# Kernel tuning notes

Hardware: AMD Instinct MI355X
Metric: run time of the kernel (lower is better)

Reference implementation:

```python
import jax, jax.numpy as jnp
import numpy as np

N_NODES = 100000


def _hetero_block(x, ei_t, ei_i, Wt, bt, Wi, bi, Wr, br):
    """ResidualGeneralHeteroConvBlock: per-edge-type linear message passing,
    'add' aggregation for temp_previous, 'mean' for intersects, summed across
    edge types, plus linear residual, ReLU."""
    n = x.shape[0]
    # transform-then-gather (cheaper than per-edge transform)
    ht = x @ Wt + bt                                   # [N, C]
    hi = x @ Wi + bi                                   # [N, C]
    # temp_previous: sum aggregation over incoming edges
    agg_t = jax.ops.segment_sum(ht[ei_t[0]], ei_t[1], num_segments=n)
    # intersects: mean aggregation
    sum_i = jax.ops.segment_sum(hi[ei_i[0]], ei_i[1], num_segments=n)
    cnt = jax.ops.segment_sum(jnp.ones((ei_i.shape[1],), x.dtype), ei_i[1],
                              num_segments=n)
    agg_i = sum_i / jnp.maximum(cnt, 1.0)[:, None]
    return jax.nn.relu(agg_t + agg_i + (x @ Wr + br))


def setup_inputs() -> dict:
    key = jax.random.key(0)
    ks = jax.random.split(key, 12)
    E = 2000000
    d = {
        "x": jax.random.normal(ks[0], (N_NODES, 6), jnp.float32),
        "edge_index_temp": jax.random.randint(ks[1], (2, E), 0, N_NODES),
        "edge_index_inter": jax.random.randint(ks[2], (2, E), 0, N_NODES),
        "W1t": jax.random.normal(ks[3], (6, 32), jnp.float32) * 0.3,
        "b1t": jnp.zeros((32,), jnp.float32),
        "W1i": jax.random.normal(ks[4], (6, 32), jnp.float32) * 0.3,
        "b1i": jnp.zeros((32,), jnp.float32),
        "W1r": jax.random.normal(ks[5], (6, 32), jnp.float32) * 0.3,
        "b1r": jnp.zeros((32,), jnp.float32),
        "W2t": jax.random.normal(ks[6], (32, 32), jnp.float32) * 0.15,
        "b2t": jnp.zeros((32,), jnp.float32),
        "W2i": jax.random.normal(ks[7], (32, 32), jnp.float32) * 0.15,
        "b2i": jnp.zeros((32,), jnp.float32),
        "W2r": jax.random.normal(ks[8], (32, 32), jnp.float32) * 0.15,
        "b2r": jnp.zeros((32,), jnp.float32),
        "Wc": jax.random.normal(ks[9], (32, 7), jnp.float32) * 0.15,
        "bc": jnp.zeros((7,), jnp.float32),
    }
    return d


def reference(x, edge_index_temp, edge_index_inter,
              W1t, b1t, W1i, b1i, W1r, b1r,
              W2t, b2t, W2i, b2i, W2r, b2r, Wc, bc):
    h = _hetero_block(x, edge_index_temp, edge_index_inter,
                      W1t, b1t, W1i, b1i, W1r, b1r)
    h = _hetero_block(h, edge_index_temp, edge_index_inter,
                      W2t, b2t, W2i, b2i, W2r, b2r)
    return h @ Wc + bc  # [N, num_classes]
```

## Files before the change

kernel.cpp:

```cpp
#include <hip/hip_runtime.h>


#define BLK 256
#define RN 512
#define KMAX 256
#define CAP 11264
#define CHUNK 4096

typedef unsigned short us8 __attribute__((ext_vector_type(8)));

__device__ inline unsigned short f2bf(float f) {
  unsigned u = __float_as_uint(f);
  return (unsigned short)((u + 0x7FFFu + ((u >> 16) & 1u)) >> 16);
}
__device__ inline float bf2f(unsigned short h) {
  return __uint_as_float(((unsigned)h) << 16);
}

__global__ __launch_bounds__(BLK) void k_prep(const float* __restrict__ x,
                                              unsigned short* __restrict__ xp,
                                              int* __restrict__ curT,
                                              int* __restrict__ curI, int N,
                                              int K) {
  int gid = blockIdx.x * BLK + threadIdx.x;
  if (gid < K) {
    curT[gid] = gid * CAP;
    curI[gid] = gid * CAP;
  }
  if (gid >= N * 8) return;
  int n = gid >> 3, c = gid & 7;
  xp[gid] = (c < 6) ? f2bf(x[n * 6 + c]) : (unsigned short)0;
}

__global__ __launch_bounds__(BLK) void k_bin3(
    const int* __restrict__ eiT, int ET, int* __restrict__ curT,
    int* __restrict__ binT, const int* __restrict__ eiI, int EI,
    int* __restrict__ curI, int* __restrict__ binI, int K) {
  const int* ei = blockIdx.y ? eiI : eiT;
  int E = blockIdx.y ? EI : ET;
  int* gcur = blockIdx.y ? curI : curT;
  int* binned = blockIdx.y ? binI : binT;
  int cs = blockIdx.x * CHUNK;
  if (cs >= E) return;
  int ce = min(E, cs + CHUNK);
  int cnt = ce - cs;
  __shared__ int ebuf[CHUNK];
  __shared__ unsigned char bbuf[CHUNK];
  __shared__ int hist[KMAX], cur[KMAX], gdelta[KMAX], s[KMAX];
  int t = threadIdx.x;
  hist[t] = 0;
  __syncthreads();
  for (int e = cs + t; e < ce; e += BLK) atomicAdd(&hist[ei[E + e] >> 9], 1);
  __syncthreads();
  int v = hist[t];
  s[t] = v;
  __syncthreads();
  for (int off = 1; off < KMAX; off <<= 1) {
    int x = (t >= off) ? s[t - off] : 0;
    __syncthreads();
    s[t] += x;
    __syncthreads();
  }
  int excl = s[t] - v;
  cur[t] = excl;
  if (t < K) gdelta[t] = atomicAdd(&gcur[t], v) - excl;
  __syncthreads();
  for (int e = cs + t; e < ce; e += BLK) {
    int src = ei[e];
    int d = ei[E + e];
    int b = d >> 9;
    int slot = atomicAdd(&cur[b], 1);
    ebuf[slot] = (src << 9) | (d & 511);
    bbuf[slot] = (unsigned char)b;
  }
  __syncthreads();
  for (int i = t; i < cnt; i += BLK) {
    int b = bbuf[i];
    __builtin_nontemporal_store(ebuf[i], &binned[i + gdelta[b]]);
  }
}

__global__ __launch_bounds__(512) void k_sortcsr4(
    const int* __restrict__ binT, const int* __restrict__ curT,
    unsigned short* __restrict__ csrT, int* __restrict__ startT,
    int* __restrict__ degT, int4* __restrict__ mqT,
    const int* __restrict__ binI, const int* __restrict__ curI,
    unsigned short* __restrict__ csrI, int* __restrict__ startI,
    int* __restrict__ degI, int4* __restrict__ mqI, int N, int qN) {
  const int* bin = blockIdx.y ? binI : binT;
  const int* cur = blockIdx.y ? curI : curT;
  unsigned short* csr = blockIdx.y ? csrI : csrT;
  int* start = blockIdx.y ? startI : startT;
  int* deg = blockIdx.y ? degI : degT;
  int4* mq = blockIdx.y ? mqI : mqT;
  __shared__ int h[4 * RN], s[RN], c2[4 * RN];
  int t = threadIdx.x, b = blockIdx.x;
  int e0 = b * CAP;
  int cnt = min(cur[b] - e0, CAP);
  h[t] = 0;
  h[t + 512] = 0;
  h[t + 1024] = 0;
  h[t + 1536] = 0;
  __syncthreads();
  for (int i = t; i < cnt; i += 512) {
    int p = bin[e0 + i];
    int src = p >> 9;
    int q = (src >= 2 * qN) ? ((src >= 3 * qN) ? 3 : 2)
                            : ((src >= qN) ? 1 : 0);
    atomicAdd(&h[((p & 511) << 2) | q], 1);
  }
  __syncthreads();
  int q0 = h[4 * t], q1 = h[4 * t + 1], q2 = h[4 * t + 2], q3 = h[4 * t + 3];
  int tot = q0 + q1 + q2 + q3;
  s[t] = tot;
  __syncthreads();
  for (int off = 1; off < 512; off <<= 1) {
    int v = (t >= off) ? s[t - off] : 0;
    __syncthreads();
    s[t] += v;
    __syncthreads();
  }
  int excl = s[t] - tot;
  c2[4 * t] = excl;
  c2[4 * t + 1] = excl + q0;
  c2[4 * t + 2] = excl + q0 + q1;
  c2[4 * t + 3] = excl + q0 + q1 + q2;
  int n = b * RN + t;
  if (n < N) {
    start[n] = e0 + excl;
    deg[n] = tot;
    mq[n] = make_int4(e0 + excl + q0, e0 + excl + q0 + q1,
                      e0 + excl + q0 + q1 + q2, 0);
  }
  __syncthreads();
  for (int i = t; i < cnt; i += 512) {
    int p = bin[e0 + i];
    int src = p >> 9;
    int q = (src >= 2 * qN) ? ((src >= 3 * qN) ? 3 : 2)
                            : ((src >= qN) ? 1 : 0);
    int key = ((p & 511) << 2) | q;
    int pos = atomicAdd(&c2[key], 1);
    csr[e0 + pos] = (unsigned short)(src - q * qN);
  }
}

#define GN1 32
__global__ __launch_bounds__(BLK) void k_g1c1(
    const unsigned short* __restrict__ xp, const float* __restrict__ x,
    const int* __restrict__ startT, const int* __restrict__ degT,
    const int4* __restrict__ mqT, const unsigned short* __restrict__ csrT,
    const int* __restrict__ startI, const int* __restrict__ degI,
    const int4* __restrict__ mqI, const unsigned short* __restrict__ csrI,
    const float* __restrict__ Wt, const float* __restrict__ bt,
    const float* __restrict__ Wi, const float* __restrict__ bi,
    const float* __restrict__ Wr, const float* __restrict__ br,
    unsigned short* __restrict__ h1b, int N, int qN) {
  __shared__ float sGT[GN1 * 32], sGI[GN1 * 32], sx[GN1 * 6];
  __shared__ float sWt[192], sWi[192], sWr[192], sb[96];
  __shared__ float sdT[GN1], sdI[GN1];
  int t = threadIdx.x, b = blockIdx.x;
  if (t < 192) { sWt[t] = Wt[t]; sWi[t] = Wi[t]; sWr[t] = Wr[t]; }
  if (t < 32) { sb[t] = bt[t]; sb[32 + t] = bi[t]; sb[64 + t] = br[t]; }
  if (t < GN1 * 6) {
    int g = b * GN1 * 6 + t;
    sx[t] = (g < N * 6) ? x[g] : 0.0f;
  }
  int nl = t >> 3, et = (t >> 2) & 1, qp = t & 3;
  int n = b * GN1 + nl;
  float a[8] = {0.f, 0.f, 0.f, 0.f, 0.f, 0.f, 0.f, 0.f};
  int d = 0;
  if (n < N) {
    const int* startA = et ? startI : startT;
    const int* degA = et ? degI : degT;
    const int4* mqA = et ? mqI : mqT;
    const unsigned short* csrA = et ? csrI : csrT;
    int s0 = startA[n];
    d = degA[n];
    int4 mv = mqA[n];
    int b0 = (qp == 0) ? s0 : ((qp == 1) ? mv.x : ((qp == 2) ? mv.y : mv.z));
    int b1 = (qp == 3) ? (s0 + d)
                       : ((qp == 0) ? mv.x : ((qp == 1) ? mv.y : mv.z));
    const unsigned short* tab = xp + (size_t)qp * qN * 8;
    int i = b0;
    for (; i + 4 <= b1; i += 4) {
      int r0 = csrA[i], r1 = csrA[i + 1], r2 = csrA[i + 2], r3 = csrA[i + 3];
      us8 v0 = *(const us8*)(tab + (size_t)r0 * 8);
      us8 v1 = *(const us8*)(tab + (size_t)r1 * 8);
      us8 v2 = *(const us8*)(tab + (size_t)r2 * 8);
      us8 v3 = *(const us8*)(tab + (size_t)r3 * 8);
#pragma unroll
      for (int k = 0; k < 8; ++k)
        a[k] += (bf2f(v0[k]) + bf2f(v1[k])) + (bf2f(v2[k]) + bf2f(v3[k]));
    }
    for (; i < b1; ++i) {
      int r0 = csrA[i];
      us8 v0 = *(const us8*)(tab + (size_t)r0 * 8);
#pragma unroll
      for (int k = 0; k < 8; ++k) a[k] += bf2f(v0[k]);
    }
  }
  float* dst = (et ? sGI : sGT) + nl * 32 + qp * 8;
#pragma unroll
  for (int k = 0; k < 8; ++k) dst[k] = a[k];
  if (qp == 0) {
    if (et) sdI[nl] = (float)d;
    else    sdT[nl] = (float)d;
  }
  __syncthreads();
  for (int idx = t; idx < GN1 * 32; idx += BLK) {
    int m = idx >> 5, j = idx & 31;
    int nn = b * GN1 + m;
    if (nn >= N) break;
    float fdT = sdT[m], fdI = sdI[m];
    float invI = 1.0f / fmaxf(fdI, 1.0f);
    float gate = (fdI > 0.0f) ? 1.0f : 0.0f;
    float acc = fdT * sb[j] + gate * sb[32 + j] + sb[64 + j];
#pragma unroll
    for (int k = 0; k < 6; ++k) {
      float gT = sGT[m * 32 + k] + sGT[m * 32 + 8 + k] +
                 sGT[m * 32 + 16 + k] + sGT[m * 32 + 24 + k];
      float gI = sGI[m * 32 + k] + sGI[m * 32 + 8 + k] +
                 sGI[m * 32 + 16 + k] + sGI[m * 32 + 24 + k];
      acc += gT * sWt[k * 32 + j];
      acc += gI * invI * sWi[k * 32 + j];
      acc += sx[m * 6 + k] * sWr[k * 32 + j];
    }
    h1b[(size_t)nn * 32 + j] = f2bf(fmaxf(acc, 0.0f));
  }
}

__device__ inline void accum8(const unsigned short* __restrict__ tab,
                              const unsigned short* __restrict__ csr, int i0,
                              int i1, float* a) {
  int i = i0;
  for (; i + 4 <= i1; i += 4) {
    int r0 = csr[i], r1 = csr[i + 1], r2 = csr[i + 2], r3 = csr[i + 3];
    us8 v0 = *(const us8*)(tab + (size_t)r0 * 32);
    us8 v1 = *(const us8*)(tab + (size_t)r1 * 32);
    us8 v2 = *(const us8*)(tab + (size_t)r2 * 32);
    us8 v3 = *(const us8*)(tab + (size_t)r3 * 32);
#pragma unroll
    for (int k = 0; k < 8; ++k)
      a[k] += (bf2f(v0[k]) + bf2f(v1[k])) + (bf2f(v2[k]) + bf2f(v3[k]));
  }
  for (; i < i1; ++i) {
    int r0 = csr[i];
    us8 v0 = *(const us8*)(tab + (size_t)r0 * 32);
#pragma unroll
    for (int k = 0; k < 8; ++k) a[k] += bf2f(v0[k]);
  }
}

__global__ __launch_bounds__(BLK) void k_gather2(
    const unsigned short* __restrict__ h1b, const int* __restrict__ startT,
    const int* __restrict__ degT, const int4* __restrict__ mqT,
    const unsigned short* __restrict__ csrT, const int* __restrict__ startI,
    const int* __restrict__ degI, const int4* __restrict__ mqI,
    const unsigned short* __restrict__ csrI, float* __restrict__ aggT,
    float* __restrict__ aggI, int N, int qN) {
  const int* start = blockIdx.y ? startI : startT;
  const int* deg = blockIdx.y ? degI : degT;
  const int4* mq = blockIdx.y ? mqI : mqT;
  const unsigned short* csr = blockIdx.y ? csrI : csrT;
  float* agg = blockIdx.y ? aggI : aggT;
  int gid = blockIdx.x * BLK + threadIdx.x;
  int n = gid >> 2;
  if (n >= N) return;
  int c8 = (gid & 3) * 8;
  float a[8] = {0.f, 0.f, 0.f, 0.f, 0.f, 0.f, 0.f, 0.f};
  int s0 = start[n], d = deg[n];
  int4 mv = mq[n];
  accum8(h1b + c8, csr, s0, mv.x, a);
  accum8(h1b + (size_t)qN * 32 + c8, csr, mv.x, mv.y, a);
  accum8(h1b + (size_t)2 * qN * 32 + c8, csr, mv.y, mv.z, a);
  accum8(h1b + (size_t)3 * qN * 32 + c8, csr, mv.z, s0 + d, a);
  float* p = agg + (size_t)n * 32 + c8;
#pragma unroll
  for (int k = 0; k < 8; ++k) __builtin_nontemporal_store(a[k], p + k);
}

#define CN 64
__global__ __launch_bounds__(BLK) void k_combine2cls(
    const float* __restrict__ aggT, const float* __restrict__ aggI,
    const unsigned short* __restrict__ h1b, const int* __restrict__ degT,
    const int* __restrict__ degI, const float* __restrict__ Wt,
    const float* __restrict__ bt, const float* __restrict__ Wi,
    const float* __restrict__ bi, const float* __restrict__ Wr,
    const float* __restrict__ br, const float* __restrict__ Wc,
    const float* __restrict__ bc, float* __restrict__ out, int N) {
  __shared__ float hTs[CN * 32], hIs[CN * 32], hRs[CN * 32], hs2[CN * 32];
  __shared__ float sWc[224], sbc[7], sb[96];
  __shared__ float sdT[CN], sdI[CN];
  int t = threadIdx.x;
  int j = t & 31, ln = t >> 5;
  float wt[32], wi[32], wr[32];
#pragma unroll
  for (int k = 0; k < 32; ++k) {
    wt[k] = Wt[k * 32 + j];
    wi[k] = Wi[k * 32 + j];
    wr[k] = Wr[k * 32 + j];
  }
  int node0 = blockIdx.x * CN;
  size_t gbase = (size_t)node0 * 32;
  {
    const float4* sT = (const float4*)(aggT + gbase);
    const float4* sI = (const float4*)(aggI + gbase);
    ((float4*)hTs)[t] = sT[t];
    ((float4*)hTs)[t + 256] = sT[t + 256];
    ((float4*)hIs)[t] = sI[t];
    ((float4*)hIs)[t + 256] = sI[t + 256];
    us8 v = ((const us8*)(h1b + gbase))[t];
    float4 lo = {bf2f(v[0]), bf2f(v[1]), bf2f(v[2]), bf2f(v[3])};
    float4 hi = {bf2f(v[4]), bf2f(v[5]), bf2f(v[6]), bf2f(v[7])};
    ((float4*)hRs)[2 * t] = lo;
    ((float4*)hRs)[2 * t + 1] = hi;
  }
  if (t < 224) sWc[t] = Wc[t];
  if (t < 7) sbc[t] = bc[t];
  if (t < 32) { sb[t] = bt[t]; sb[32 + t] = bi[t]; sb[64 + t] = br[t]; }
  if (t < CN) {
    int n = node0 + t;
    sdT[t] = (n < N) ? (float)degT[n] : 0.f;
    sdI[t] = (n < N) ? (float)degI[n] : 0.f;
  }
  __syncthreads();
#pragma unroll
  for (int it = 0; it < CN / 8; ++it) {
    int li = it * 8 + ln;
    float dT = sdT[li], dI = sdI[li];
    float invI = 1.0f / fmaxf(dI, 1.0f);
    float gate = (dI > 0.0f) ? 1.0f : 0.0f;
    float aT = 0.f, aI = 0.f, aR = 0.f;
    const float4* hT4 = (const float4*)(hTs + li * 32);
    const float4* hI4 = (const float4*)(hIs + li * 32);
    const float4* hR4 = (const float4*)(hRs + li * 32);
#pragma unroll
    for (int kk = 0; kk < 8; ++kk) {
      float4 a = hT4[kk], bI = hI4[kk], r = hR4[kk];
      aT += a.x * wt[kk * 4 + 0] + a.y * wt[kk * 4 + 1] +
            a.z * wt[kk * 4 + 2] + a.w * wt[kk * 4 + 3];
      aI += bI.x * wi[kk * 4 + 0] + bI.y * wi[kk * 4 + 1] +
            bI.z * wi[kk * 4 + 2] + bI.w * wi[kk * 4 + 3];
      aR += r.x * wr[kk * 4 + 0] + r.y * wr[kk * 4 + 1] +
            r.z * wr[kk * 4 + 2] + r.w * wr[kk * 4 + 3];
    }
    float acc = dT * sb[j] + gate * sb[32 + j] + sb[64 + j] + aT + invI * aI + aR;
    hs2[li * 32 + j] = fmaxf(acc, 0.0f);
  }
  __syncthreads();
  if (t < 224) {
#pragma unroll
    for (int pass = 0; pass < CN * 7 / 224; ++pass) {
      int o = pass * 224 + t;
      int m = o / 7, jc = o - m * 7;
      int n = node0 + m;
      if (n < N) {
        float a = sbc[jc];
        const float* hp = hs2 + m * 32;
#pragma unroll
        for (int k = 0; k < 32; ++k) a += hp[k] * sWc[k * 7 + jc];
        out[(size_t)n * 7 + jc] = a;
      }
    }
  }
}

extern "C" void kernel_launch(void* const* d_in, const int* in_sizes, int n_in,
                              void* d_out, int out_size, void* d_ws,
                              size_t ws_size, hipStream_t stream) {
  const float* x   = (const float*)d_in[0];
  const int* ei_t  = (const int*)d_in[1];
  const int* ei_i  = (const int*)d_in[2];
  const float* W1t = (const float*)d_in[3];
  const float* b1t = (const float*)d_in[4];
  const float* W1i = (const float*)d_in[5];
  const float* b1i = (const float*)d_in[6];
  const float* W1r = (const float*)d_in[7];
  const float* b1r = (const float*)d_in[8];
  const float* W2t = (const float*)d_in[9];
  const float* b2t = (const float*)d_in[10];
  const float* W2i = (const float*)d_in[11];
  const float* b2i = (const float*)d_in[12];
  const float* W2r = (const float*)d_in[13];
  const float* b2r = (const float*)d_in[14];
  const float* Wc  = (const float*)d_in[15];
  const float* bc  = (const float*)d_in[16];
  float* out = (float*)d_out;

  const int N  = in_sizes[0] / 6;
  const int E  = in_sizes[1] / 2;
  const int Ei = in_sizes[2] / 2;
  const int K  = (N + RN - 1) / RN;
  const int qN = (N + 3) >> 2;

  float* aggT = (float*)d_ws;
  float* aggI = aggT + (size_t)N * 32;
  int4* mqT   = (int4*)(aggI + (size_t)N * 32);
  int4* mqI   = mqT + N;
  unsigned short* h1b = (unsigned short*)(mqI + N);
  unsigned short* xp  = h1b + (size_t)N * 32;
  int* curT   = (int*)(xp + (size_t)N * 8);
  int* curI   = curT + KMAX;
  int* startT = curI + KMAX;
  int* degT   = startT + N;
  int* startI = degT + N;
  int* degI   = startI + N;
  int* binT   = degI + N;
  int* binI   = binT + (size_t)K * CAP;
  unsigned short* csrT = (unsigned short*)(binI + (size_t)K * CAP);
  unsigned short* csrI = csrT + (size_t)K * CAP;

  const int gN8  = (N * 8 + BLK - 1) / BLK;
  const int gG1  = (N + GN1 - 1) / GN1;
  const int gG2  = (N * 4 + BLK - 1) / BLK;
  const int gC2  = (N + CN - 1) / CN;
  const int Emax = (E > Ei) ? E : Ei;
  const int gBin = (Emax + CHUNK - 1) / CHUNK;

  k_prep<<<gN8, BLK, 0, stream>>>(x, xp, curT, curI, N, K);
  k_bin3<<<dim3(gBin, 2), BLK, 0, stream>>>(ei_t, E, curT, binT, ei_i, Ei,
                                            curI, binI, K);
  k_sortcsr4<<<dim3(K, 2), 512, 0, stream>>>(binT, curT, csrT, startT, degT,
                                             mqT, binI, curI, csrI, startI,
                                             degI, mqI, N, qN);

  k_g1c1<<<gG1, BLK, 0, stream>>>(xp, x, startT, degT, mqT, csrT, startI,
                                  degI, mqI, csrI, W1t, b1t, W1i, b1i, W1r,
                                  b1r, h1b, N, qN);

  k_gather2<<<dim3(gG2, 2), BLK, 0, stream>>>(h1b, startT, degT, mqT, csrT,
                                              startI, degI, mqI, csrI, aggT,
                                              aggI, N, qN);
  k_combine2cls<<<gC2, BLK, 0, stream>>>(aggT, aggI, h1b, degT, degI, W2t,
                                         b2t, W2i, b2i, W2r, b2r, Wc, bc, out,
                                         N);
}
```

Measured before the change: 257.1 us.

## Sort nodes by degree within each bin to balance gather work across lanes

Adds a per-bin counting sort of nodes by in-degree (per edge type in the CSR build, and by combined degree in a new small kernel). The gather kernels then process nodes in this order so that threads in one wavefront have similar edge counts, which reduces divergence and tail imbalance. The cost is an extra kernel launch, extra shared-memory scans, and an indirection through the order array. It also scatters the node writes in k_gather2 and k_g1c1 instead of writing them contiguously.

```diff
diff --git a/kernel.cpp b/kernel.cpp
--- a/kernel.cpp
+++ b/kernel.cpp
@@ -83,17 +83,20 @@
 __global__ __launch_bounds__(512) void k_sortcsr4(
     const int* __restrict__ binT, const int* __restrict__ curT,
     unsigned short* __restrict__ csrT, int* __restrict__ startT,
-    int* __restrict__ degT, int4* __restrict__ mqT,
+    int* __restrict__ degT, int4* __restrict__ mqT, int* __restrict__ ordT,
     const int* __restrict__ binI, const int* __restrict__ curI,
     unsigned short* __restrict__ csrI, int* __restrict__ startI,
-    int* __restrict__ degI, int4* __restrict__ mqI, int N, int qN) {
+    int* __restrict__ degI, int4* __restrict__ mqI, int* __restrict__ ordI,
+    int N, int qN) {
   const int* bin = blockIdx.y ? binI : binT;
   const int* cur = blockIdx.y ? curI : curT;
   unsigned short* csr = blockIdx.y ? csrI : csrT;
   int* start = blockIdx.y ? startI : startT;
   int* deg = blockIdx.y ? degI : degT;
   int4* mq = blockIdx.y ? mqI : mqT;
+  int* ord = blockIdx.y ? ordI : ordT;
   __shared__ int h[4 * RN], s[RN], c2[4 * RN];
+  __shared__ int dh[128], dcur[128];
   int t = threadIdx.x, b = blockIdx.x;
   int e0 = b * CAP;
   int cnt = min(cur[b] - e0, CAP);
@@ -126,7 +129,8 @@
   c2[4 * t + 2] = excl + q0 + q1;
   c2[4 * t + 3] = excl + q0 + q1 + q2;
   int n = b * RN + t;
-  if (n < N) {
+  bool valid = (n < N);
+  if (valid) {
     start[n] = e0 + excl;
     deg[n] = tot;
     mq[n] = make_int4(e0 + excl + q0, e0 + excl + q0 + q1,
@@ -142,6 +146,56 @@
     int pos = atomicAdd(&c2[key], 1);
     csr[e0 + pos] = (unsigned short)(src - q * qN);
   }
+  if (t < 128) dh[t] = 0;
+  __syncthreads();
+  int dc = min(tot, 127);
+  if (valid) atomicAdd(&dh[dc], 1);
+  __syncthreads();
+  if (t < 128) s[t] = dh[t];
+  __syncthreads();
+  for (int off = 1; off < 128; off <<= 1) {
+    int v = (t >= off && t < 128) ? s[t - off] : 0;
+    __syncthreads();
+    if (t < 128) s[t] += v;
+    __syncthreads();
+  }
+  if (t < 128) dcur[t] = s[t] - dh[t];
+  __syncthreads();
+  if (valid) {
+    int r = atomicAdd(&dcur[dc], 1);
+    ord[b * RN + r] = n;
+  }
+}
+
+__global__ __launch_bounds__(512) void k_ordc(const int* __restrict__ degT,
+                                              const int* __restrict__ degI,
+                                              int* __restrict__ ordC, int N) {
+  __shared__ int dh[256], s2[256], dcur[256];
+  int t = threadIdx.x, b = blockIdx.x;
+  int n = b * 512 + t;
+  if (t < 256) dh[t] = 0;
+  __syncthreads();
+  bool valid = (n < N);
+  int dc = 0;
+  if (valid) {
+    dc = min(degT[n] + degI[n], 255);
+    atomicAdd(&dh[dc], 1);
+  }
+  __syncthreads();
+  if (t < 256) s2[t] = dh[t];
+  __syncthreads();
+  for (int off = 1; off < 256; off <<= 1) {
+    int v = (t >= off && t < 256) ? s2[t - off] : 0;
+    __syncthreads();
+    if (t < 256) s2[t] += v;
+    __syncthreads();
+  }
+  if (t < 256) dcur[t] = s2[t] - dh[t];
+  __syncthreads();
+  if (valid) {
+    int r = atomicAdd(&dcur[dc], 1);
+    ordC[b * 512 + r] = n;
+  }
 }
 
 #define GN1 32
@@ -151,25 +205,33 @@
     const int4* __restrict__ mqT, const unsigned short* __restrict__ csrT,
     const int* __restrict__ startI, const int* __restrict__ degI,
     const int4* __restrict__ mqI, const unsigned short* __restrict__ csrI,
-    const float* __restrict__ Wt, const float* __restrict__ bt,
-    const float* __restrict__ Wi, const float* __restrict__ bi,
-    const float* __restrict__ Wr, const float* __restrict__ br,
-    unsigned short* __restrict__ h1b, int N, int qN) {
+    const int* __restrict__ ordC, const float* __restrict__ Wt,
+    const float* __restrict__ bt, const float* __restrict__ Wi,
+    const float* __restrict__ bi, const float* __restrict__ Wr,
+    const float* __restrict__ br, unsigned short* __restrict__ h1b, int N,
+    int qN) {
   __shared__ float sGT[GN1 * 32], sGI[GN1 * 32], sx[GN1 * 6];
   __shared__ float sWt[192], sWi[192], sWr[192], sb[96];
   __shared__ float sdT[GN1], sdI[GN1];
+  __shared__ int snid[GN1];
   int t = threadIdx.x, b = blockIdx.x;
   if (t < 192) { sWt[t] = Wt[t]; sWi[t] = Wi[t]; sWr[t] = Wr[t]; }
   if (t < 32) { sb[t] = bt[t]; sb[32 + t] = bi[t]; sb[64 + t] = br[t]; }
+  if (t < GN1) {
+    int g = b * GN1 + t;
+    snid[t] = (g < N) ? ordC[g] : -1;
+  }
+  __syncthreads();
   if (t < GN1 * 6) {
-    int g = b * GN1 * 6 + t;
-    sx[t] = (g < N * 6) ? x[g] : 0.0f;
+    int m = t / 6, c = t - m * 6;
+    int nn = snid[m];
+    sx[t] = (nn >= 0) ? x[nn * 6 + c] : 0.0f;
   }
   int nl = t >> 3, et = (t >> 2) & 1, qp = t & 3;
-  int n = b * GN1 + nl;
+  int n = snid[nl];
   float a[8] = {0.f, 0.f, 0.f, 0.f, 0.f, 0.f, 0.f, 0.f};
   int d = 0;
-  if (n < N) {
+  if (n >= 0) {
     const int* startA = et ? startI : startT;
     const int* degA = et ? degI : degT;
     const int4* mqA = et ? mqI : mqT;
@@ -209,8 +271,8 @@
   __syncthreads();
   for (int idx = t; idx < GN1 * 32; idx += BLK) {
     int m = idx >> 5, j = idx & 31;
-    int nn = b * GN1 + m;
-    if (nn >= N) break;
+    int nn = snid[m];
+    if (nn < 0) continue;
     float fdT = sdT[m], fdI = sdI[m];
     float invI = 1.0f / fmaxf(fdI, 1.0f);
     float gate = (fdI > 0.0f) ? 1.0f : 0.0f;
@@ -256,16 +318,19 @@
     const int* __restrict__ degT, const int4* __restrict__ mqT,
     const unsigned short* __restrict__ csrT, const int* __restrict__ startI,
     const int* __restrict__ degI, const int4* __restrict__ mqI,
-    const unsigned short* __restrict__ csrI, float* __restrict__ aggT,
+    const unsigned short* __restrict__ csrI, const int* __restrict__ ordT,
+    const int* __restrict__ ordI, float* __restrict__ aggT,
     float* __restrict__ aggI, int N, int qN) {
   const int* start = blockIdx.y ? startI : startT;
   const int* deg = blockIdx.y ? degI : degT;
   const int4* mq = blockIdx.y ? mqI : mqT;
   const unsigned short* csr = blockIdx.y ? csrI : csrT;
+  const int* ord = blockIdx.y ? ordI : ordT;
   float* agg = blockIdx.y ? aggI : aggT;
   int gid = blockIdx.x * BLK + threadIdx.x;
-  int n = gid >> 2;
-  if (n >= N) return;
+  int n0 = gid >> 2;
+  if (n0 >= N) return;
+  int n = ord[n0];
   int c8 = (gid & 3) * 8;
   float a[8] = {0.f, 0.f, 0.f, 0.f, 0.f, 0.f, 0.f, 0.f};
   int s0 = start[n], d = deg[n];
@@ -405,7 +470,10 @@
   int* degT   = startT + N;
   int* startI = degT + N;
   int* degI   = startI + N;
-  int* binT   = degI + N;
+  int* ordT   = degI + N;
+  int* ordI   = ordT + N;
+  int* ordC   = ordI + N;
+  int* binT   = ordC + N;
   int* binI   = binT + (size_t)K * CAP;
   unsigned short* csrT = (unsigned short*)(binI + (size_t)K * CAP);
   unsigned short* csrI = csrT + (size_t)K * CAP;
@@ -421,16 +489,17 @@
   k_bin3<<<dim3(gBin, 2), BLK, 0, stream>>>(ei_t, E, curT, binT, ei_i, Ei,
                                             curI, binI, K);
   k_sortcsr4<<<dim3(K, 2), 512, 0, stream>>>(binT, curT, csrT, startT, degT,
-                                             mqT, binI, curI, csrI, startI,
-                                             degI, mqI, N, qN);
+                                             mqT, ordT, binI, curI, csrI,
+                                             startI, degI, mqI, ordI, N, qN);
+  k_ordc<<<K, 512, 0, stream>>>(degT, degI, ordC, N);
 
   k_g1c1<<<gG1, BLK, 0, stream>>>(xp, x, startT, degT, mqT, csrT, startI,
-                                  degI, mqI, csrI, W1t, b1t, W1i, b1i, W1r,
-                                  b1r, h1b, N, qN);
+                                  degI, mqI, csrI, ordC, W1t, b1t, W1i, b1i,
+                                  W1r, b1r, h1b, N, qN);
 
   k_gather2<<<dim3(gG2, 2), BLK, 0, stream>>>(h1b, startT, degT, mqT, csrT,
-                                              startI, degI, mqI, csrI, aggT,
-                                              aggI, N, qN);
+                                              startI, degI, mqI, csrI, ordT,
+                                              ordI, aggT, aggI, N, qN);
   k_combine2cls<<<gC2, BLK, 0, stream>>>(aggT, aggI, h1b, degT, degI, W2t,
                                          b2t, W2i, b2i, W2r, b2r, Wc, bc, out,
                                          N);
```

After: 281.2 us. +9.4%, slower.
